# Optimization experiments

Measured on AMD Instinct MI355X. Metric: run time of the kernel, lower is better.

Reference implementation:

```python
import jax, jax.numpy as jnp
import numpy as np

B, N, CHANNELS = 4, 2048, 512
HEADS, HEAD_DIM = 8, 64
HIDDEN = HEADS * HEAD_DIM
ROPE_THETA = 10000.0


def _rotate_half(x):
    # interleaved pairs, as in rotary_embedding_torch
    x1 = x[..., 0::2]
    x2 = x[..., 1::2]
    return jnp.stack((-x2, x1), axis=-1).reshape(x.shape)


def _rope(x):
    # x: [b, h, n, d]; rotate over seq axis -2, full head dim
    n, d = x.shape[-2], x.shape[-1]
    inv_freq = 1.0 / (ROPE_THETA ** (jnp.arange(0, d, 2, dtype=jnp.float32) / d))
    freqs = jnp.arange(n, dtype=jnp.float32)[:, None] * inv_freq  # [n, d/2]
    freqs = jnp.repeat(freqs, 2, axis=-1)  # [n, d]
    return x * jnp.cos(freqs) + _rotate_half(x) * jnp.sin(freqs)


def setup_inputs() -> dict:
    key = jax.random.key(0)
    k1, k2, k3, k4 = jax.random.split(key, 4)
    x = jax.random.normal(k1, (B, N, CHANNELS), dtype=jnp.float32)
    pos_bias = jax.random.normal(k2, (HEADS, N, N), dtype=jnp.float32) * 0.02
    w_qkv = jax.random.normal(k3, (3 * HIDDEN, CHANNELS), dtype=jnp.float32) / np.sqrt(CHANNELS)
    w_out = jax.random.normal(k4, (CHANNELS, HIDDEN), dtype=jnp.float32) / np.sqrt(HIDDEN)
    return {"x": x, "pos_bias": pos_bias, "w_qkv": w_qkv, "w_out": w_out}


def reference(x, pos_bias, w_qkv, w_out):
    scale = HEAD_DIM ** -0.5
    b, n, _ = x.shape
    qkv = x @ w_qkv.T  # [b, n, 3*hidden]
    q, k, v = jnp.split(qkv, 3, axis=-1)

    def split_heads(z):
        return z.reshape(b, n, HEADS, HEAD_DIM).transpose(0, 2, 1, 3)  # [b,h,n,d]

    q, k, v = map(split_heads, (q, k, v))
    q = q * scale
    q = _rope(q)
    k = _rope(k)
    sim = jnp.einsum('bhid,bhjd->bhij', q, k) + pos_bias  # pos_bias [h,n,n] broadcasts
    attn = jax.nn.softmax(sim, axis=-1)  # matches sim - amax(detached) then softmax
    out = jnp.einsum('bhij,bhjd->bhid', attn, v)
    out = out.transpose(0, 2, 1, 3).reshape(b, n, HIDDEN)
    return out @ w_out.T
```

## Files before the change

kernel.cpp:

```cpp
#include <hip/hip_runtime.h>
#include <hip/hip_bf16.h>
#include <math.h>

typedef __bf16 bf16;
typedef bf16  bf16x8 __attribute__((ext_vector_type(8)));
typedef bf16  bf16x4 __attribute__((ext_vector_type(4)));
typedef float f32x4  __attribute__((ext_vector_type(4)));
typedef float f32x16 __attribute__((ext_vector_type(16)));

#define B_   4
#define N_   2048
#define CH_  512
#define H_   8
#define D_   64
#define HID_ 512

__device__ __forceinline__ f32x4 mfma16(bf16x8 a, bf16x8 b, f32x4 c) {
    return __builtin_amdgcn_mfma_f32_16x16x32_bf16(a, b, c, 0, 0, 0);
}
__device__ __forceinline__ f32x16 mfma32(bf16x8 a, bf16x8 b, f32x16 c) {
    return __builtin_amdgcn_mfma_f32_32x32x16_bf16(a, b, c, 0, 0, 0);
}

__global__ void rope_table_k(float* __restrict__ cosT, float* __restrict__ sinT) {
    int idx = blockIdx.x * 256 + threadIdx.x;
    int pos = idx >> 5, fi = idx & 31;
    double inv = pow(10000.0, -(double)(2 * fi) / 64.0);
    double ang = (double)pos * inv;
    cosT[idx] = (float)cos(ang);
    sinT[idx] = (float)sin(ang);
}

__global__ __launch_bounds__(256) void qkv_rope_k(
    const float* __restrict__ x, const float* __restrict__ w,
    const float* __restrict__ cosT, const float* __restrict__ sinT,
    bf16* __restrict__ Qb, bf16* __restrict__ Kb, bf16* __restrict__ Vt)
{
    __shared__ __align__(16) bf16 Xs[128][40];
    __shared__ __align__(16) bf16 Ws[128][40];
    const int tid = threadIdx.x, lane = tid & 63, wid = tid >> 6;
    const int wr = wid >> 1, wc = wid & 1;
    const int m0 = blockIdx.x * 128, n0 = blockIdx.y * 128;
    const int l15 = lane & 15, l4 = lane >> 4;
    const int sr = tid >> 1, sh = (tid & 1) * 16;

    f32x4 acc[4][4] = {};

    for (int kt = 0; kt < 16; ++kt) {
        __syncthreads();
        {
            const float4* xp = reinterpret_cast<const float4*>(x + (size_t)(m0 + sr) * CH_ + kt * 32 + sh);
            const float4* wp = reinterpret_cast<const float4*>(w + (size_t)(n0 + sr) * CH_ + kt * 32 + sh);
#pragma unroll
            for (int j = 0; j < 4; ++j) {
                float4 f = xp[j];
                bf16x4 o1 = { (bf16)f.x, (bf16)f.y, (bf16)f.z, (bf16)f.w };
                *reinterpret_cast<bf16x4*>(&Xs[sr][sh + j * 4]) = o1;
                float4 g = wp[j];
                bf16x4 o2 = { (bf16)g.x, (bf16)g.y, (bf16)g.z, (bf16)g.w };
                *reinterpret_cast<bf16x4*>(&Ws[sr][sh + j * 4]) = o2;
            }
        }
        __syncthreads();
        bf16x8 a[4], bb[4];
#pragma unroll
        for (int mf = 0; mf < 4; ++mf)
            a[mf] = *reinterpret_cast<const bf16x8*>(&Xs[wr * 64 + mf * 16 + l15][l4 * 8]);
#pragma unroll
        for (int nf = 0; nf < 4; ++nf)
            bb[nf] = *reinterpret_cast<const bf16x8*>(&Ws[wc * 64 + nf * 16 + l15][l4 * 8]);
#pragma unroll
        for (int mf = 0; mf < 4; ++mf)
#pragma unroll
            for (int nf = 0; nf < 4; ++nf)
                acc[mf][nf] = mfma16(a[mf], bb[nf], acc[mf][nf]);
    }

#pragma unroll
    for (int nf = 0; nf < 4; ++nf) {
        const int col = n0 + wc * 64 + nf * 16 + l15;
        const int sec = col >> 9;
        const int cc = col & 511;
        const int hh = cc >> 6, dd = cc & 63;
        if (sec == 2) {
#pragma unroll
            for (int mf = 0; mf < 4; ++mf) {
                const int pos0 = m0 + wr * 64 + mf * 16 + l4 * 4;
                const int bb_ = pos0 >> 11, pos = pos0 & 2047;
                bf16x4 pk = { (bf16)acc[mf][nf][0], (bf16)acc[mf][nf][1],
                              (bf16)acc[mf][nf][2], (bf16)acc[mf][nf][3] };
                *reinterpret_cast<bf16x4*>(
                    Vt + ((size_t)(bb_ * H_ + hh) * D_ + dd) * N_ + pos) = pk;
            }
        } else {
            const float sgn = (dd & 1) ? 1.f : -1.f;
#pragma unroll
            for (int mf = 0; mf < 4; ++mf) {
#pragma unroll
                for (int i = 0; i < 4; ++i) {
                    const int row = m0 + wr * 64 + mf * 16 + l4 * 4 + i;
                    const int bb_ = row >> 11, pos = row & 2047;
                    const float v = acc[mf][nf][i];
                    const float v2 = __shfl_xor(v, 1);
                    const size_t dst = ((size_t)((bb_ * H_ + hh) * N_ + pos)) * D_ + dd;
                    const float c = cosT[pos * 32 + (dd >> 1)];
                    const float s = sinT[pos * 32 + (dd >> 1)];
                    const float r = v * c + sgn * v2 * s;
                    if (sec == 0) Qb[dst] = (bf16)(r * 0.125f);
                    else          Kb[dst] = (bf16)r;
                }
            }
        }
    }
}

#define KRD2(kt2,kc) (((kt2)*32 + l31)*128 + (((kc)*32 + l5*16) ^ (l7<<4)))
#define VRD2(dt,kt)  (((dt)*32 + l31)*128 + (((kt)*32 + l5*16) ^ (l7<<4)))
#define PRD2(kt)     (wid*4096 + l31*128 + (((kt)*32 + l5*16) ^ (l7<<4)))
#define PST2(kt2,r2) (wid*4096 + l31*128 + (((kt2)*64 + (r2)*16 + l5*8) ^ (l7<<4)))

__global__ __launch_bounds__(128, 2) void attn_k(
    const bf16* __restrict__ Qb, const bf16* __restrict__ Kb, const bf16* __restrict__ Vt,
    const float* __restrict__ bias, bf16* __restrict__ AO)
{
    __shared__ __align__(16) unsigned char KsB[2][8192];
    __shared__ __align__(16) unsigned char VsB[2][8192];
    __shared__ __align__(16) unsigned char PwB[2][4096];

    const int tid = threadIdx.x, lane = tid & 63, wid = tid >> 6;
    const int l31 = lane & 31, l5 = lane >> 5, l7 = lane & 7;
    const int id = blockIdx.x;
    const int xcd = id & 7, j = id >> 3;
    const int bh = xcd + 8 * (j >> 5);
    const int qt = j & 31;
    const int b = bh >> 3, h = bh & 7;
    const int q0 = qt * 64 + wid * 32;
    const size_t bhoff = (size_t)bh * N_ * D_;

    bf16x8 qreg[4];
#pragma unroll
    for (int kc = 0; kc < 4; ++kc)
        qreg[kc] = *reinterpret_cast<const bf16x8*>(
            Qb + bhoff + (size_t)(q0 + l31) * D_ + kc * 16 + l5 * 8);

    const unsigned scol = ((lane & 7) * 16) ^ ((lane >> 3) << 4);
    const char* kg = (const char*)(Kb + bhoff) + (size_t)(wid * 32 + (lane >> 3)) * 128 + scol;
    const char* vg = (const char*)(Vt + bhoff) + (size_t)(wid * 32 + (lane >> 3)) * (N_ * 2) + scol;

    const float* bp = bias + ((size_t)h * N_ + (q0 + l31)) * N_ + l5 * 4;

    unsigned char* pwD = &PwB[0][0];

#define GLL(src, dst) __builtin_amdgcn_global_load_lds( \
        (const __attribute__((address_space(1))) unsigned int*)(src), \
        (__attribute__((address_space(3))) unsigned int*)(dst), 16, 0, 0)

#define STAGE(buf, t) do { \
        GLL(kg + (size_t)(t) * 8192,            &KsB[buf][wid * 4096]); \
        GLL(kg + (size_t)(t) * 8192 + 1024,     &KsB[buf][wid * 4096 + 1024]); \
        GLL(kg + (size_t)(t) * 8192 + 2048,     &KsB[buf][wid * 4096 + 2048]); \
        GLL(kg + (size_t)(t) * 8192 + 3072,     &KsB[buf][wid * 4096 + 3072]); \
        GLL(vg + (size_t)(t) * 128,             &VsB[buf][wid * 4096]); \
        GLL(vg + (size_t)(t) * 128 + 32768,     &VsB[buf][wid * 4096 + 1024]); \
        GLL(vg + (size_t)(t) * 128 + 65536,     &VsB[buf][wid * 4096 + 2048]); \
        GLL(vg + (size_t)(t) * 128 + 98304,     &VsB[buf][wid * 4096 + 3072]); \
    } while (0)

#define PIPE_SYNC() do { \
        asm volatile("s_waitcnt vmcnt(8)" ::: "memory"); \
        __builtin_amdgcn_sched_barrier(0); \
        __builtin_amdgcn_s_barrier(); \
        __builtin_amdgcn_sched_barrier(0); \
    } while (0)

    f32x16 o[2] = {};
    float lp = 0.f;
    f32x4 bc[2][4], bn[2][4];

    STAGE(0, 0);
    __builtin_amdgcn_sched_barrier(0);
#pragma unroll
    for (int kt2 = 0; kt2 < 2; ++kt2)
#pragma unroll
        for (int r2 = 0; r2 < 4; ++r2)
            bc[kt2][r2] = *reinterpret_cast<const f32x4*>(bp + kt2 * 32 + r2 * 8);
    PIPE_SYNC();

#pragma unroll 2
    for (int kb = 0; kb < 32; ++kb) {
        const int cur = kb & 1;
        if (kb < 31) {
            STAGE(cur ^ 1, kb + 1);
            __builtin_amdgcn_sched_barrier(0);
#pragma unroll
            for (int kt2 = 0; kt2 < 2; ++kt2)
#pragma unroll
                for (int r2 = 0; r2 < 4; ++r2)
                    bn[kt2][r2] = *reinterpret_cast<const f32x4*>(
                        bp + (size_t)(kb + 1) * 64 + kt2 * 32 + r2 * 8);
        }

        const unsigned char* ksC = &KsB[cur][0];
        f32x16 s[2] = {};
        __builtin_amdgcn_s_setprio(1);
#pragma unroll
        for (int kt2 = 0; kt2 < 2; ++kt2) {
#pragma unroll
            for (int kc = 0; kc < 4; ++kc) {
                bf16x8 kf = *reinterpret_cast<const bf16x8*>(ksC + KRD2(kt2, kc));
                s[kt2] = mfma32(kf, qreg[kc], s[kt2]);
            }
        }
        __builtin_amdgcn_s_setprio(0);

#pragma unroll
        for (int kt2 = 0; kt2 < 2; ++kt2) {
#pragma unroll
            for (int r2 = 0; r2 < 4; ++r2) {
                float p0 = __expf(s[kt2][r2 * 4 + 0] + bc[kt2][r2][0]);
                float p1 = __expf(s[kt2][r2 * 4 + 1] + bc[kt2][r2][1]);
                float p2 = __expf(s[kt2][r2 * 4 + 2] + bc[kt2][r2][2]);
                float p3 = __expf(s[kt2][r2 * 4 + 3] + bc[kt2][r2][3]);
                lp += (p0 + p1) + (p2 + p3);
                bf16x4 pk = { (bf16)p0, (bf16)p1, (bf16)p2, (bf16)p3 };
                *reinterpret_cast<bf16x4*>(pwD + PST2(kt2, r2)) = pk;
            }
        }

        const unsigned char* vsC = &VsB[cur][0];
        __builtin_amdgcn_s_setprio(1);
#pragma unroll
        for (int kt = 0; kt < 4; ++kt) {
            bf16x8 pa = *reinterpret_cast<const bf16x8*>(pwD + PRD2(kt));
#pragma unroll
            for (int dt = 0; dt < 2; ++dt) {
                bf16x8 vf = *reinterpret_cast<const bf16x8*>(vsC + VRD2(dt, kt));
                o[dt] = mfma32(pa, vf, o[dt]);
            }
        }
        __builtin_amdgcn_s_setprio(0);

#pragma unroll
        for (int kt2 = 0; kt2 < 2; ++kt2)
#pragma unroll
            for (int r2 = 0; r2 < 4; ++r2)
                bc[kt2][r2] = bn[kt2][r2];

        PIPE_SYNC();
    }

    float tot = lp;
    tot += __shfl_xor(tot, 32);
    float rv[16];
#pragma unroll
    for (int reg = 0; reg < 16; ++reg) {
        const int qr = (reg & 3) + 8 * (reg >> 2) + 4 * l5;
        rv[reg] = 1.0f / __shfl(tot, qr);
    }
#pragma unroll
    for (int dt = 0; dt < 2; ++dt)
#pragma unroll
        for (int reg = 0; reg < 16; ++reg) {
            const int qr = (reg & 3) + 8 * (reg >> 2) + 4 * l5;
            AO[((size_t)(b * N_ + q0 + qr)) * HID_ + h * D_ + dt * 32 + l31] =
                (bf16)(o[dt][reg] * rv[reg]);
        }
}

__global__ __launch_bounds__(256) void proj_k(
    const bf16* __restrict__ A, const float* __restrict__ w, float* __restrict__ out)
{
    __shared__ __align__(16) bf16 As[128][40];
    __shared__ __align__(16) bf16 Ws[128][40];
    const int tid = threadIdx.x, lane = tid & 63, wid = tid >> 6;
    const int wr = wid >> 1, wc = wid & 1;
    const int m0 = blockIdx.x * 128, n0 = blockIdx.y * 128;
    const int l15 = lane & 15, l4 = lane >> 4;
    const int sr = tid >> 1, sh = (tid & 1) * 16;

    f32x4 acc[4][4] = {};

    for (int kt = 0; kt < 16; ++kt) {
        __syncthreads();
        {
            const bf16* ap = A + (size_t)(m0 + sr) * HID_ + kt * 32 + sh;
            *reinterpret_cast<bf16x8*>(&As[sr][sh])     = *reinterpret_cast<const bf16x8*>(ap);
            *reinterpret_cast<bf16x8*>(&As[sr][sh + 8]) = *reinterpret_cast<const bf16x8*>(ap + 8);
            const float4* wp = reinterpret_cast<const float4*>(w + (size_t)(n0 + sr) * HID_ + kt * 32 + sh);
#pragma unroll
            for (int j = 0; j < 4; ++j) {
                float4 g = wp[j];
                bf16x4 o2 = { (bf16)g.x, (bf16)g.y, (bf16)g.z, (bf16)g.w };
                *reinterpret_cast<bf16x4*>(&Ws[sr][sh + j * 4]) = o2;
            }
        }
        __syncthreads();
        bf16x8 a[4], bb[4];
#pragma unroll
        for (int mf = 0; mf < 4; ++mf)
            a[mf] = *reinterpret_cast<const bf16x8*>(&As[wr * 64 + mf * 16 + l15][l4 * 8]);
#pragma unroll
        for (int nf = 0; nf < 4; ++nf)
            bb[nf] = *reinterpret_cast<const bf16x8*>(&Ws[wc * 64 + nf * 16 + l15][l4 * 8]);
#pragma unroll
        for (int mf = 0; mf < 4; ++mf)
#pragma unroll
            for (int nf = 0; nf < 4; ++nf)
                acc[mf][nf] = mfma16(a[mf], bb[nf], acc[mf][nf]);
    }
#pragma unroll
    for (int nf = 0; nf < 4; ++nf) {
        const int col = n0 + wc * 64 + nf * 16 + l15;
#pragma unroll
        for (int mf = 0; mf < 4; ++mf) {
#pragma unroll
            for (int i = 0; i < 4; ++i) {
                const int row = m0 + wr * 64 + mf * 16 + l4 * 4 + i;
                out[(size_t)row * HID_ + col] = acc[mf][nf][i];
            }
        }
    }
}

extern "C" void kernel_launch(void* const* d_in, const int* in_sizes, int n_in,
                              void* d_out, int out_size, void* d_ws, size_t ws_size,
                              hipStream_t stream) {
    (void)in_sizes; (void)n_in; (void)out_size; (void)ws_size;
    const float* x     = (const float*)d_in[0];
    const float* bias  = (const float*)d_in[1];
    const float* w_qkv = (const float*)d_in[2];
    const float* w_out = (const float*)d_in[3];
    float* out = (float*)d_out;

    bf16* Qb = (bf16*)d_ws;
    bf16* Kb = Qb + 4194304;
    bf16* Vt = Kb + 4194304;
    bf16* AO = Vt + 4194304;
    float* cosT = (float*)(AO + 4194304);
    float* sinT = cosT + 65536;

    rope_table_k<<<dim3(256), 256, 0, stream>>>(cosT, sinT);
    qkv_rope_k  <<<dim3(64, 12), 256, 0, stream>>>(x, w_qkv, cosT, sinT, Qb, Kb, Vt);
    attn_k      <<<dim3(1024), 128, 0, stream>>>(Qb, Kb, Vt, bias, AO);
    proj_k      <<<dim3(64, 4), 256, 0, stream>>>(AO, w_out, out);
}
```

Before: 154.6 us.

## Keep P in registers via lane shuffles and prefetch bias two tiles ahead

```diff
diff --git a/kernel.cpp b/kernel.cpp
--- a/kernel.cpp
+++ b/kernel.cpp
@@ -7,6 +7,8 @@
 typedef bf16  bf16x4 __attribute__((ext_vector_type(4)));
 typedef float f32x4  __attribute__((ext_vector_type(4)));
 typedef float f32x16 __attribute__((ext_vector_type(16)));
+typedef unsigned int u32x2 __attribute__((ext_vector_type(2)));
+typedef unsigned int u32x4 __attribute__((ext_vector_type(4)));
 
 #define B_   4
 #define N_   2048
@@ -116,8 +118,6 @@
 
 #define KRD2(kt2,kc) (((kt2)*32 + l31)*128 + (((kc)*32 + l5*16) ^ (l7<<4)))
 #define VRD2(dt,kt)  (((dt)*32 + l31)*128 + (((kt)*32 + l5*16) ^ (l7<<4)))
-#define PRD2(kt)     (wid*4096 + l31*128 + (((kt)*32 + l5*16) ^ (l7<<4)))
-#define PST2(kt2,r2) (wid*4096 + l31*128 + (((kt2)*64 + (r2)*16 + l5*8) ^ (l7<<4)))
 
 __global__ __launch_bounds__(128, 2) void attn_k(
     const bf16* __restrict__ Qb, const bf16* __restrict__ Kb, const bf16* __restrict__ Vt,
@@ -125,7 +125,6 @@
 {
     __shared__ __align__(16) unsigned char KsB[2][8192];
     __shared__ __align__(16) unsigned char VsB[2][8192];
-    __shared__ __align__(16) unsigned char PwB[2][4096];
 
     const int tid = threadIdx.x, lane = tid & 63, wid = tid >> 6;
     const int l31 = lane & 31, l5 = lane >> 5, l7 = lane & 7;
@@ -148,8 +147,6 @@
     const char* vg = (const char*)(Vt + bhoff) + (size_t)(wid * 32 + (lane >> 3)) * (N_ * 2) + scol;
 
     const float* bp = bias + ((size_t)h * N_ + (q0 + l31)) * N_ + l5 * 4;
-
-    unsigned char* pwD = &PwB[0][0];
 
 #define GLL(src, dst) __builtin_amdgcn_global_load_lds( \
         (const __attribute__((address_space(1))) unsigned int*)(src), \
@@ -175,15 +172,17 @@
 
     f32x16 o[2] = {};
     float lp = 0.f;
-    f32x4 bc[2][4], bn[2][4];
+    f32x4 bc[2][4], bn[2][4], b2[2][4];
 
     STAGE(0, 0);
     __builtin_amdgcn_sched_barrier(0);
 #pragma unroll
     for (int kt2 = 0; kt2 < 2; ++kt2)
 #pragma unroll
-        for (int r2 = 0; r2 < 4; ++r2)
+        for (int r2 = 0; r2 < 4; ++r2) {
             bc[kt2][r2] = *reinterpret_cast<const f32x4*>(bp + kt2 * 32 + r2 * 8);
+            bn[kt2][r2] = *reinterpret_cast<const f32x4*>(bp + 64 + kt2 * 32 + r2 * 8);
+        }
     PIPE_SYNC();
 
 #pragma unroll 2
@@ -192,12 +191,14 @@
         if (kb < 31) {
             STAGE(cur ^ 1, kb + 1);
             __builtin_amdgcn_sched_barrier(0);
+        }
+        if (kb < 30) {
 #pragma unroll
             for (int kt2 = 0; kt2 < 2; ++kt2)
 #pragma unroll
                 for (int r2 = 0; r2 < 4; ++r2)
-                    bn[kt2][r2] = *reinterpret_cast<const f32x4*>(
-                        bp + (size_t)(kb + 1) * 64 + kt2 * 32 + r2 * 8);
+                    b2[kt2][r2] = *reinterpret_cast<const f32x4*>(
+                        bp + (size_t)(kb + 2) * 64 + kt2 * 32 + r2 * 8);
         }
 
         const unsigned char* ksC = &KsB[cur][0];
@@ -213,8 +214,10 @@
         }
         __builtin_amdgcn_s_setprio(0);
 
+        bf16x8 pa[4];
 #pragma unroll
         for (int kt2 = 0; kt2 < 2; ++kt2) {
+            unsigned U[4][2], R[4][2];
 #pragma unroll
             for (int r2 = 0; r2 < 4; ++r2) {
                 float p0 = __expf(s[kt2][r2 * 4 + 0] + bc[kt2][r2][0]);
@@ -223,7 +226,24 @@
                 float p3 = __expf(s[kt2][r2 * 4 + 3] + bc[kt2][r2][3]);
                 lp += (p0 + p1) + (p2 + p3);
                 bf16x4 pk = { (bf16)p0, (bf16)p1, (bf16)p2, (bf16)p3 };
-                *reinterpret_cast<bf16x4*>(pwD + PST2(kt2, r2)) = pk;
+                u32x2 uu = __builtin_bit_cast(u32x2, pk);
+                U[r2][0] = uu[0];
+                U[r2][1] = uu[1];
+            }
+#pragma unroll
+            for (int r2 = 0; r2 < 4; ++r2) {
+                R[r2][0] = __shfl_xor(U[r2][0], 32);
+                R[r2][1] = __shfl_xor(U[r2][1], 32);
+            }
+            const bool hi = (l5 != 0);
+#pragma unroll
+            for (int ktp = 0; ktp < 2; ++ktp) {
+                unsigned g0 = hi ? R[2 * ktp + 1][0] : U[2 * ktp][0];
+                unsigned g1 = hi ? R[2 * ktp + 1][1] : U[2 * ktp][1];
+                unsigned h0 = hi ? U[2 * ktp + 1][0] : R[2 * ktp][0];
+                unsigned h1 = hi ? U[2 * ktp + 1][1] : R[2 * ktp][1];
+                u32x4 wv = { g0, g1, h0, h1 };
+                pa[kt2 * 2 + ktp] = __builtin_bit_cast(bf16x8, wv);
             }
         }
 
@@ -231,11 +251,10 @@
         __builtin_amdgcn_s_setprio(1);
 #pragma unroll
         for (int kt = 0; kt < 4; ++kt) {
-            bf16x8 pa = *reinterpret_cast<const bf16x8*>(pwD + PRD2(kt));
 #pragma unroll
             for (int dt = 0; dt < 2; ++dt) {
                 bf16x8 vf = *reinterpret_cast<const bf16x8*>(vsC + VRD2(dt, kt));
-                o[dt] = mfma32(pa, vf, o[dt]);
+                o[dt] = mfma32(pa[kt], vf, o[dt]);
             }
         }
         __builtin_amdgcn_s_setprio(0);
@@ -243,8 +262,10 @@
 #pragma unroll
         for (int kt2 = 0; kt2 < 2; ++kt2)
 #pragma unroll
-            for (int r2 = 0; r2 < 4; ++r2)
+            for (int r2 = 0; r2 < 4; ++r2) {
                 bc[kt2][r2] = bn[kt2][r2];
+                bn[kt2][r2] = b2[kt2][r2];
+            }
 
         PIPE_SYNC();
     }
```

Measured after the change: 156.4 us. Within noise of the previous version (+1.1%).

## Pack two batch items per attention block so blocks share pos_bias locality

Applied to the files above, without the earlier changes.

```diff
diff --git a/kernel.cpp b/kernel.cpp
--- a/kernel.cpp
+++ b/kernel.cpp
@@ -116,26 +116,27 @@
 
 #define KRD2(kt2,kc) (((kt2)*32 + l31)*128 + (((kc)*32 + l5*16) ^ (l7<<4)))
 #define VRD2(dt,kt)  (((dt)*32 + l31)*128 + (((kt)*32 + l5*16) ^ (l7<<4)))
-#define PRD2(kt)     (wid*4096 + l31*128 + (((kt)*32 + l5*16) ^ (l7<<4)))
-#define PST2(kt2,r2) (wid*4096 + l31*128 + (((kt2)*64 + (r2)*16 + l5*8) ^ (l7<<4)))
-
-__global__ __launch_bounds__(128, 2) void attn_k(
+#define PRD2(kt)     (l31*128 + (((kt)*32 + l5*16) ^ (l7<<4)))
+#define PST2(kt2,r2) (l31*128 + (((kt2)*64 + (r2)*16 + l5*8) ^ (l7<<4)))
+
+__global__ __launch_bounds__(256, 2) void attn_k(
     const bf16* __restrict__ Qb, const bf16* __restrict__ Kb, const bf16* __restrict__ Vt,
     const float* __restrict__ bias, bf16* __restrict__ AO)
 {
-    __shared__ __align__(16) unsigned char KsB[2][8192];
-    __shared__ __align__(16) unsigned char VsB[2][8192];
-    __shared__ __align__(16) unsigned char PwB[2][4096];
-
-    const int tid = threadIdx.x, lane = tid & 63, wid = tid >> 6;
+    __shared__ __align__(16) unsigned char KsB[2][2][8192];
+    __shared__ __align__(16) unsigned char VsB[2][2][8192];
+    __shared__ __align__(16) unsigned char PwB[4][4096];
+
+    const int tid = threadIdx.x, lane = tid & 63, ww = tid >> 6;
     const int l31 = lane & 31, l5 = lane >> 5, l7 = lane & 7;
+    const int wb = ww >> 1;
+    const int w  = ww & 1;
     const int id = blockIdx.x;
-    const int xcd = id & 7, j = id >> 3;
-    const int bh = xcd + 8 * (j >> 5);
-    const int qt = j & 31;
-    const int b = bh >> 3, h = bh & 7;
-    const int q0 = qt * 64 + wid * 32;
-    const size_t bhoff = (size_t)bh * N_ * D_;
+    const int h = id & 7, j = id >> 3;
+    const int bp = j & 1, qt = j >> 1;
+    const int b = bp * 2 + wb;
+    const int q0 = qt * 64 + w * 32;
+    const size_t bhoff = (size_t)(b * H_ + h) * N_ * D_;
 
     bf16x8 qreg[4];
 #pragma unroll
@@ -143,27 +144,28 @@
         qreg[kc] = *reinterpret_cast<const bf16x8*>(
             Qb + bhoff + (size_t)(q0 + l31) * D_ + kc * 16 + l5 * 8);
 
-    const unsigned scol = ((lane & 7) * 16) ^ ((lane >> 3) << 4);
-    const char* kg = (const char*)(Kb + bhoff) + (size_t)(wid * 32 + (lane >> 3)) * 128 + scol;
-    const char* vg = (const char*)(Vt + bhoff) + (size_t)(wid * 32 + (lane >> 3)) * (N_ * 2) + scol;
-
-    const float* bp = bias + ((size_t)h * N_ + (q0 + l31)) * N_ + l5 * 4;
-
-    unsigned char* pwD = &PwB[0][0];
+    const unsigned kcol = ((lane & 7) * 16) ^ ((lane >> 3) << 4);
+    const char* sgK = (const char*)(Kb + bhoff) + (size_t)(lane >> 3) * 128 + kcol;
+    const char* sgV = (const char*)(Vt + bhoff) + (size_t)(lane >> 3) * (N_ * 2) + kcol;
+    const char* sg = w ? sgV : sgK;
+    const size_t tstep = w ? (size_t)128 : (size_t)8192;
+    const size_t gstep = w ? (size_t)8 * N_ * 2 : (size_t)1024;
+    unsigned char* sdB = w ? &VsB[wb][0][0] : &KsB[wb][0][0];
+
+    const float* bpp = bias + ((size_t)h * N_ + (q0 + l31)) * N_ + l5 * 4;
+
+    unsigned char* pwD = &PwB[ww][0];
 
 #define GLL(src, dst) __builtin_amdgcn_global_load_lds( \
         (const __attribute__((address_space(1))) unsigned int*)(src), \
         (__attribute__((address_space(3))) unsigned int*)(dst), 16, 0, 0)
 
 #define STAGE(buf, t) do { \
-        GLL(kg + (size_t)(t) * 8192,            &KsB[buf][wid * 4096]); \
-        GLL(kg + (size_t)(t) * 8192 + 1024,     &KsB[buf][wid * 4096 + 1024]); \
-        GLL(kg + (size_t)(t) * 8192 + 2048,     &KsB[buf][wid * 4096 + 2048]); \
-        GLL(kg + (size_t)(t) * 8192 + 3072,     &KsB[buf][wid * 4096 + 3072]); \
-        GLL(vg + (size_t)(t) * 128,             &VsB[buf][wid * 4096]); \
-        GLL(vg + (size_t)(t) * 128 + 32768,     &VsB[buf][wid * 4096 + 1024]); \
-        GLL(vg + (size_t)(t) * 128 + 65536,     &VsB[buf][wid * 4096 + 2048]); \
-        GLL(vg + (size_t)(t) * 128 + 98304,     &VsB[buf][wid * 4096 + 3072]); \
+        const char* _s = sg + (size_t)(t) * tstep; \
+        unsigned char* _d = sdB + (size_t)(buf) * 8192; \
+        _Pragma("unroll") \
+        for (int g = 0; g < 8; ++g) \
+            GLL(_s + (size_t)g * gstep, _d + g * 1024); \
     } while (0)
 
 #define PIPE_SYNC() do { \
@@ -183,7 +185,7 @@
     for (int kt2 = 0; kt2 < 2; ++kt2)
 #pragma unroll
         for (int r2 = 0; r2 < 4; ++r2)
-            bc[kt2][r2] = *reinterpret_cast<const f32x4*>(bp + kt2 * 32 + r2 * 8);
+            bc[kt2][r2] = *reinterpret_cast<const f32x4*>(bpp + kt2 * 32 + r2 * 8);
     PIPE_SYNC();
 
 #pragma unroll 2
@@ -197,10 +199,10 @@
 #pragma unroll
                 for (int r2 = 0; r2 < 4; ++r2)
                     bn[kt2][r2] = *reinterpret_cast<const f32x4*>(
-                        bp + (size_t)(kb + 1) * 64 + kt2 * 32 + r2 * 8);
-        }
-
-        const unsigned char* ksC = &KsB[cur][0];
+                        bpp + (size_t)(kb + 1) * 64 + kt2 * 32 + r2 * 8);
+        }
+
+        const unsigned char* ksC = &KsB[wb][cur][0];
         f32x16 s[2] = {};
         __builtin_amdgcn_s_setprio(1);
 #pragma unroll
@@ -227,7 +229,7 @@
             }
         }
 
-        const unsigned char* vsC = &VsB[cur][0];
+        const unsigned char* vsC = &VsB[wb][cur][0];
         __builtin_amdgcn_s_setprio(1);
 #pragma unroll
         for (int kt = 0; kt < 4; ++kt) {
@@ -341,6 +343,6 @@
 
     rope_table_k<<<dim3(256), 256, 0, stream>>>(cosT, sinT);
     qkv_rope_k  <<<dim3(64, 12), 256, 0, stream>>>(x, w_qkv, cosT, sinT, Qb, Kb, Vt);
-    attn_k      <<<dim3(1024), 128, 0, stream>>>(Qb, Kb, Vt, bias, AO);
+    attn_k      <<<dim3(512), 256, 0, stream>>>(Qb, Kb, Vt, bias, AO);
     proj_k      <<<dim3(64, 4), 256, 0, stream>>>(AO, w_out, out);
 }
```

New measurement: 165.0 us. +6.7%, slower.
